# Optimization experiments

Measured on AMD Instinct MI355X. Metric: run time of the kernel, lower is better.

The kernel has to match this reference:

```python
import jax, jax.numpy as jnp
import numpy as np

B, T, D, V, L = 16, 1024, 512, 256, 64
INF = jnp.float32(1e30)


def _dp(reps, codebook):
    # per-frame squared L2 distance to each codebook token: (B, T, V)
    d = (jnp.sum(reps * reps, -1, keepdims=True)
         - 2.0 * jnp.einsum('btd,vd->btv', reps, codebook)
         + jnp.sum(codebook * codebook, -1))
    # cumulative cost table: C[:, t] = sum of distances of first t frames, C[:,0]=0
    C = jnp.concatenate([jnp.zeros((B, 1, V), d.dtype), jnp.cumsum(d, axis=1)], axis=1)

    def step(costs, t):
        start = jnp.maximum(t - L, 0)
        s_idx = start + jnp.arange(L)                          # candidate segment starts
        Ct = jax.lax.dynamic_slice(C, (0, t, 0), (B, 1, V))    # (B,1,V)
        Cw = jax.lax.dynamic_slice(C, (0, start, 0), (B, L, V))
        seg = Ct - Cw                                          # (B,L,V): cost of segment (s, t] per token
        seg_tok = jnp.argmin(seg, axis=-1)                     # best token per start
        seg_cost = jnp.take_along_axis(seg, seg_tok[..., None], axis=-1)[..., 0]
        cw = jax.lax.dynamic_slice(costs, (0, start), (B, L))
        total = jnp.where((s_idx < t)[None, :], cw + seg_cost, INF)
        idx = jnp.argmin(total, axis=1)                        # best start within window
        val = jnp.take_along_axis(total, idx[:, None], 1)[:, 0]
        tok = jnp.take_along_axis(seg_tok, idx[:, None], 1)[:, 0]
        prev = start + idx
        costs = jax.lax.dynamic_update_slice(costs, val[:, None], (0, t))
        return costs, (prev.astype(jnp.int32), tok.astype(jnp.int32))

    costs0 = jnp.zeros((B, T + 1), d.dtype)
    costs, (prev_t, tok_t) = jax.lax.scan(step, costs0, jnp.arange(1, T + 1))
    prev = jnp.zeros((B, T + 1), jnp.int32).at[:, 1:].set(prev_t.T)
    tokens = jnp.zeros((B, T + 1), jnp.int32).at[:, 1:].set(tok_t.T)
    return costs, prev, tokens


def _backtrack(prev, tokens, lengths):
    bidx = jnp.arange(B)

    def step(st, _):
        active = st > 0
        bnd = jnp.where(active, st, 0)
        tk = jnp.where(active, tokens[bidx, st], 0)
        st_new = jnp.where(active, prev[bidx, st], 0)
        return st_new, (bnd, tk, active)

    _, (bs, ts, act) = jax.lax.scan(step, lengths, None, length=T)
    bs, ts, act = bs.T, ts.T, act.T                            # (B,T), back-to-front order
    counts = jnp.sum(act.astype(jnp.int32), axis=1)
    ridx = counts[:, None] - 1 - jnp.arange(T)[None, :]        # reverse to front-to-back
    valid = ridx >= 0
    ridx = jnp.clip(ridx, 0, T - 1)
    boundaries = jnp.where(valid, jnp.take_along_axis(bs, ridx, 1), 0)
    label_tokens = jnp.where(valid, jnp.take_along_axis(ts, ridx, 1), 0)
    return boundaries, label_tokens, counts


def setup_inputs() -> dict:
    key = jax.random.key(0)
    k1, k2, k3 = jax.random.split(key, 3)
    reps = jax.random.normal(k1, (B, T, D), dtype=jnp.float32)
    codebook = jax.random.normal(k2, (V, D), dtype=jnp.float32)
    lengths = jax.random.randint(k3, (B,), T // 2, T + 1, dtype=jnp.int32)
    return {"reps": reps, "codebook": codebook, "lengths": lengths}


def reference(reps, codebook, lengths):
    lengths = jnp.minimum(lengths, T).astype(jnp.int32)
    costs, prev, tokens = _dp(reps, codebook)
    boundaries, label_tokens, counts = _backtrack(prev, tokens, lengths)
    final_costs = costs[jnp.arange(B), lengths]
    return boundaries, label_tokens, counts, final_costs
```

## Files before the change

kernel.cpp:

```cpp
#include <hip/hip_runtime.h>

#define BB 16
#define TT 1024
#define DD 512
#define VV 256
#define MM (BB*TT)

#define DPINF 1e30f

typedef __attribute__((ext_vector_type(8))) short bf16x8;
typedef __attribute__((ext_vector_type(4))) float f32x4;

#define DPP_MIN_STEP(m, CTRL) { \
  int _t = __builtin_amdgcn_update_dpp(__float_as_int(m), __float_as_int(m), CTRL, 0xF, 0xF, false); \
  m = fminf(m, __int_as_float(_t)); }

#define DPP_MIN_REDUCE(m) \
  DPP_MIN_STEP(m, 0x111); DPP_MIN_STEP(m, 0x112); DPP_MIN_STEP(m, 0x114); \
  DPP_MIN_STEP(m, 0x118); DPP_MIN_STEP(m, 0x142); DPP_MIN_STEP(m, 0x143);

__global__ __launch_bounds__(256) void fill_k(int4* __restrict__ Wf) {
  size_t i = (size_t)blockIdx.x * 256 + threadIdx.x;
  Wf[i] = make_int4(0x7F7F7F7F, 0x7F7F7F7F, 0x7F7F7F7F, 0x7F7F7F7F);
}

__global__ __launch_bounds__(256) void norms_k(const float* __restrict__ reps,
                                               const float* __restrict__ cb,
                                               float* __restrict__ r2,
                                               float* __restrict__ c2,
                                               ushort* __restrict__ repsb,
                                               ushort* __restrict__ cbb) {
  int row = blockIdx.x * 4 + (threadIdx.x >> 6);
  int lane = threadIdx.x & 63;
  const float* src;
  float* dst;
  ushort* bdst;
  if (row < MM) {
    src = reps + (size_t)row * DD;
    dst = r2 + row;
    bdst = repsb + (size_t)row * DD;
  } else {
    int r = row - MM;
    if (r >= VV) return;
    src = cb + (size_t)r * DD;
    dst = c2 + r;
    bdst = cbb + (size_t)r * DD;
  }
  const float4* s4 = (const float4*)src;
  float4 a = s4[lane];
  float4 b = s4[lane + 64];

  auto cvt = [](float x) -> ushort {
    unsigned u = __float_as_uint(x);
    return (ushort)((u + 0x7FFFu + ((u >> 16) & 1u)) >> 16);
  };
  ushort4 ua = make_ushort4(cvt(a.x), cvt(a.y), cvt(a.z), cvt(a.w));
  ushort4 ub = make_ushort4(cvt(b.x), cvt(b.y), cvt(b.z), cvt(b.w));
  *(ushort4*)&bdst[lane * 4] = ua;
  *(ushort4*)&bdst[256 + lane * 4] = ub;

  float s = a.x*a.x + a.y*a.y + a.z*a.z + a.w*a.w
          + b.x*b.x + b.y*b.y + b.z*b.z + b.w*b.w;
#pragma unroll
  for (int off = 1; off < 64; off <<= 1) s += __shfl_xor(s, off);
  if (lane == 0) *dst = s;
}

__global__ __launch_bounds__(256) void gemm_k(const ushort* __restrict__ repsb,
                                              const ushort* __restrict__ cbb,
                                              const float* __restrict__ r2,
                                              const float* __restrict__ c2,
                                              float* __restrict__ dmat) {
  __shared__ short Ab[2][4096];
  __shared__ short Bb[2][4096];
  int tid = threadIdx.x;
  int w = tid >> 6, l = tid & 63;
  int m0 = blockIdx.x * 64, v0 = blockIdx.y * 64;

  int srow = l >> 3;
  int scol = ((l & 7) << 4) ^ (srow << 4);

  auto stage = [&](int buf, int kc) {
#pragma unroll
    for (int ii = 0; ii < 2; ++ii) {
      int instr = w + ii * 4;
      int row = instr * 8 + srow;
      const char* ga = (const char*)repsb + ((size_t)(m0 + row) * DD + kc * 64) * 2 + scol;
      __builtin_amdgcn_global_load_lds((const unsigned int*)ga,
                                       (unsigned int*)&Ab[buf][instr * 512], 16, 0, 0);
      const char* gb = (const char*)cbb + ((size_t)(v0 + row) * DD + kc * 64) * 2 + scol;
      __builtin_amdgcn_global_load_lds((const unsigned int*)gb,
                                       (unsigned int*)&Bb[buf][instr * 512], 16, 0, 0);
    }
  };

  int fr = l & 15;
  int fq = l >> 4;
  int swz = (fr & 7) << 3;

  f32x4 acc0 = {0.f,0.f,0.f,0.f}, acc1 = {0.f,0.f,0.f,0.f};
  f32x4 acc2 = {0.f,0.f,0.f,0.f}, acc3 = {0.f,0.f,0.f,0.f};

  stage(0, 0);
  int cur = 0;
  for (int kc = 0; kc < 8; ++kc) {
    if (kc < 7) {
      stage(cur ^ 1, kc + 1);
      asm volatile("s_waitcnt vmcnt(4)" ::: "memory");
    } else {
      asm volatile("s_waitcnt vmcnt(0)" ::: "memory");
    }
    __syncthreads();
#pragma unroll
    for (int ks = 0; ks < 2; ++ks) {
      int koff = (ks * 32 + fq * 8) ^ swz;
      bf16x8 av = *(const bf16x8*)&Ab[cur][(w * 16 + fr) * 64 + koff];
      bf16x8 b0 = *(const bf16x8*)&Bb[cur][(0 * 16 + fr) * 64 + koff];
      bf16x8 b1 = *(const bf16x8*)&Bb[cur][(1 * 16 + fr) * 64 + koff];
      bf16x8 b2 = *(const bf16x8*)&Bb[cur][(2 * 16 + fr) * 64 + koff];
      bf16x8 b3 = *(const bf16x8*)&Bb[cur][(3 * 16 + fr) * 64 + koff];
      acc0 = __builtin_amdgcn_mfma_f32_16x16x32_bf16(av, b0, acc0, 0, 0, 0);
      acc1 = __builtin_amdgcn_mfma_f32_16x16x32_bf16(av, b1, acc1, 0, 0, 0);
      acc2 = __builtin_amdgcn_mfma_f32_16x16x32_bf16(av, b2, acc2, 0, 0, 0);
      acc3 = __builtin_amdgcn_mfma_f32_16x16x32_bf16(av, b3, acc3, 0, 0, 0);
    }
    __syncthreads();
    cur ^= 1;
  }

  float rv[4];
#pragma unroll
  for (int r = 0; r < 4; ++r) rv[r] = r2[m0 + w * 16 + fq * 4 + r];
#pragma unroll
  for (int vt = 0; vt < 4; ++vt) {
    f32x4 a = (vt == 0) ? acc0 : (vt == 1) ? acc1 : (vt == 2) ? acc2 : acc3;
    int v = v0 + vt * 16 + fr;
    float cc = c2[v];
#pragma unroll
    for (int r = 0; r < 4; ++r) {
      int m = m0 + w * 16 + fq * 4 + r;
      dmat[(size_t)m * VV + v] = fmaf(-2.f, a[r], rv[r] + cc);
    }
  }
}

__global__ __launch_bounds__(256, 4) void w_k(const float* __restrict__ dmat,
                                              int* __restrict__ Wf) {
  __shared__ __align__(16) float CL[128 * 64];
  __shared__ __align__(16) float TOT[16 * 64];
  int bx = blockIdx.x;
  int b = bx >> 6;
  int chunk = (bx >> 2) & 15;
  int q = bx & 3;
  int t1 = 1 + (chunk << 6);
  int tid = threadIdx.x;
  int wv = tid >> 6, lane = tid & 63;

  {
    int c = tid >> 4;
    int g = tid & 15;
    const float* base = dmat + (size_t)b * TT * VV + q * 64 + (g << 2);
    float4 rr[8];
    float4 run = make_float4(0.f, 0.f, 0.f, 0.f);
#pragma unroll
    for (int jj = 1; jj <= 8; ++jj) {
      int k = (c << 3) + jj;
      int f = t1 - 64 + k;
      bool valid = (k <= 127) && (f >= 1) && (f <= TT);
      int fc = valid ? f : 1;
      float4 dv = *(const float4*)(base + (size_t)(fc - 1) * VV);
      if (!valid) dv = make_float4(0.f, 0.f, 0.f, 0.f);
      run.x += dv.x; run.y += dv.y; run.z += dv.z; run.w += dv.w;
      rr[jj - 1] = run;
    }
    *(float4*)&TOT[(c << 6) + (g << 2)] = run;
    if (c == 0) *(float4*)&CL[(g << 2)] = make_float4(0.f, 0.f, 0.f, 0.f);
    __syncthreads();
    float4 off = make_float4(0.f, 0.f, 0.f, 0.f);
#pragma unroll
    for (int cc = 0; cc < 15; ++cc) {
      if (cc < c) {
        float4 tv = *(const float4*)&TOT[(cc << 6) + (g << 2)];
        off.x += tv.x; off.y += tv.y; off.z += tv.z; off.w += tv.w;
      }
    }
#pragma unroll
    for (int jj = 1; jj <= 8; ++jj) {
      int k = (c << 3) + jj;
      if (k <= 127) {
        float4 s = rr[jj - 1];
        s.x += off.x; s.y += off.y; s.z += off.z; s.w += off.w;
        *(float4*)&CL[(k << 6) + ((g ^ (k & 15)) << 2)] = s;
      }
    }
  }
  __syncthreads();

  float bw[16];
#pragma unroll
  for (int j = 0; j < 16; ++j) {
    int dt = (j << 2) + wv;
    int ks = dt + lane;
    int kt = dt + 64;
    int rti = __float_as_int(CL[(kt << 6) + (((lane >> 2) ^ (kt & 15)) << 2) + (lane & 3)]);
    int ksm = ks & 15;
    const float* rs = &CL[ks << 6];
    float bv = 1e38f;
#pragma unroll
    for (int g = 0; g < 16; ++g) {
      float4 a = *(const float4*)&rs[(g ^ ksm) << 2];
      int v0 = g << 2;
      float t0 = __int_as_float(__builtin_amdgcn_readlane(rti, v0));
      float t1v = __int_as_float(__builtin_amdgcn_readlane(rti, v0 + 1));
      float t2 = __int_as_float(__builtin_amdgcn_readlane(rti, v0 + 2));
      float t3 = __int_as_float(__builtin_amdgcn_readlane(rti, v0 + 3));
      float m01 = fminf(t0 - a.x, t1v - a.y);
      float m23 = fminf(t2 - a.z, t3 - a.w);
      bv = fminf(bv, fminf(m01, m23));
    }
    bw[j] = bv;
  }

  __syncthreads();
  float* ST = CL;
#pragma unroll
  for (int j = 0; j < 16; ++j) {
    int dt = (j << 2) + wv;
    int srow = dt + lane;
    ST[(63 - lane) * 127 + srow] = bw[j];
  }
  __syncthreads();
  {
    int* Wfb = Wf + (size_t)b * TT * 64;
    for (int qq = 0; qq < 32; ++qq) {
      int rr = wv * 32 + qq;
      if (rr > 126) break;
      int s = t1 - 64 + rr;
      if (s < 0) continue;
      int jlo = 63 - rr; if (jlo < 0) jlo = 0;
      int jhi = 126 - rr; if (jhi > 63) jhi = 63;
      int j = lane;
      if (j >= jlo && j <= jhi)
        atomicMin(&Wfb[(size_t)s * 64 + j], __float_as_int(ST[j * 127 + rr]));
    }
  }
}

__global__ __launch_bounds__(64) void dp_seq(const float* __restrict__ Wf,
                                             float* __restrict__ cg) {
  __shared__ __align__(16) float ring[256 * 64];
  int b = blockIdx.x;
  int lane = threadIdx.x;
  const char* Wb = (const char*)(Wf + (size_t)b * TT * 64);
  float* cgb = cg + (size_t)b * (TT + 1);
  if (lane == 0) cgb[0] = 0.f;

  auto stage4 = [&](int d) {
    const char* g = Wb + ((size_t)d << 10) + (lane << 4);
    __builtin_amdgcn_global_load_lds((const unsigned int*)g,
                                     (unsigned int*)&ring[((d << 2) & 255) << 6], 16, 0, 0);
  };
  auto ldring = [&](int r) -> float {
    int rc = (r > TT - 1) ? (TT - 1) : r;
    return ring[((rc & 255) << 6) | ((lane - rc) & 63)];
  };

  for (int d = 0; d < 60; ++d) stage4(d);
  asm volatile("s_waitcnt vmcnt(56)" ::: "memory");
  float p0 = ldring(0), p1 = ldring(1), p2 = ldring(2), p3 = ldring(3);
  float p4 = ldring(4), p5 = ldring(5), p6 = ldring(6), p7 = ldring(7);

  float c = 0.f;
  float acc = DPINF;
  float ckeep = 0.f;

#define STEP(TAU, P) { \
    float cand = c + (P); \
    acc = fminf(acc, cand); \
    int fl = (TAU) & 63; \
    float cnew = __int_as_float(__builtin_amdgcn_readlane(__float_as_int(acc), fl)); \
    bool me = (lane == fl); \
    ckeep = me ? cnew : ckeep; \
    acc = me ? DPINF : acc; \
    c = cnew; }

  for (int gg = 0; gg < 16; ++gg) {
#pragma unroll
    for (int ii = 0; ii < 8; ++ii) {
      int tb = gg * 64 + ii * 8;
      if (tb <= 776) {
        asm volatile("s_waitcnt vmcnt(56)" ::: "memory");
        stage4(60 + (tb >> 2)); stage4(61 + (tb >> 2));
      } else if (tb == 784) {
        asm volatile("s_waitcnt vmcnt(0)" ::: "memory");
      }
      STEP(tb + 0, p0); p0 = ldring(tb + 8);
      STEP(tb + 1, p1); p1 = ldring(tb + 9);
      STEP(tb + 2, p2); p2 = ldring(tb + 10);
      STEP(tb + 3, p3); p3 = ldring(tb + 11);
      STEP(tb + 4, p4); p4 = ldring(tb + 12);
      STEP(tb + 5, p5); p5 = ldring(tb + 13);
      STEP(tb + 6, p6); p6 = ldring(tb + 14);
      STEP(tb + 7, p7); p7 = ldring(tb + 15);
    }
    cgb[gg * 64 + 1 + lane] = ckeep;
  }
#undef STEP
}

__global__ __launch_bounds__(256) void prev_k(const float* __restrict__ Wf,
                                              const float* __restrict__ cg,
                                              int* __restrict__ pk) {
  __shared__ float WL[127 * 64];
  int bx = blockIdx.x;
  int b = bx >> 4;
  int chunk = bx & 15;
  int t0 = chunk << 6;
  int tid = threadIdx.x;
  int wv = tid >> 6, lane = tid & 63;

  const float* Wfb = Wf + (size_t)b * TT * 64;
  for (int ci = tid; ci < 127 * 16; ci += 256) {
    int row = ci >> 4, c4 = ci & 15;
    long s = (long)(t0 - 63 + row);
    float4 v = *(const float4*)(Wfb + s * 64 + (c4 << 2));
    *(float4*)&WL[(row << 6) + (c4 << 2)] = v;
  }
  __syncthreads();

  const float* cgb = cg + (size_t)b * (TT + 1);
#pragma unroll
  for (int u = 0; u < 16; ++u) {
    int tt = wv * 16 + u;
    int t = t0 + 1 + tt;
    int i = lane;
    int s = t - 64 + i;
    float wval = WL[(tt + i) * 64 + (63 - i)];
    int sc = (s < 0) ? 0 : s;
    float total = (s >= 0) ? (cgb[sc] + wval) : DPINF;
    float m = total;
    DPP_MIN_REDUCE(m);
    float mf = __int_as_float(__builtin_amdgcn_readlane(__float_as_int(m), 63));
    unsigned long long msk = __ballot(total == mf);
    int iwin = __builtin_ctzll(msk);
    int prev = t - 64 + iwin;
    if (lane == 0) pk[(size_t)b * (TT + 1) + t] = prev;
  }
}

__global__ __launch_bounds__(64) void bt_k(const int* __restrict__ pk,
                                           const float* __restrict__ cg,
                                           const int* __restrict__ lengths,
                                           float* __restrict__ out) {
  __shared__ ushort J[10][TT + 1];
  int b = blockIdx.x;
  int lane = threadIdx.x;
  const int* pb = pk + (size_t)b * (TT + 1);

  for (int t = lane; t <= TT; t += 64)
    J[0][t] = (ushort)((t == 0) ? 0 : pb[t]);
  __syncthreads();
#pragma unroll
  for (int k = 0; k < 9; ++k) {
    for (int t = lane; t <= TT; t += 64)
      J[k + 1][t] = J[k][J[k][t]];
    __syncthreads();
  }

  int len = lengths[b];
  len = (len > TT) ? TT : (len < 0 ? 0 : len);

  int cnt = 0;
  if (len > 0) {
    int cur = len, m = 0;
#pragma unroll
    for (int k = 9; k >= 0; --k) {
      int nxt = J[k][cur];
      if (nxt != 0) { cur = nxt; m += (1 << k); }
    }
    cnt = m + 1;
  }

  float* bout = out + b * TT;
  float* tout = out + MM + b * TT;
#pragma unroll 4
  for (int j0 = 0; j0 < TT; j0 += 64) {
    int j = j0 + lane;
    int node = 0;
    if (j < cnt) {
      int steps = cnt - 1 - j;
      int cur = len;
#pragma unroll
      for (int k = 9; k >= 0; --k)
        if ((steps >> k) & 1) cur = J[k][cur];
      node = cur;
    }
    bout[j] = (float)node;
    tout[j] = 0.f;
  }
  if (lane == 0) {
    out[2 * MM + b] = (float)cnt;
    out[2 * MM + BB + b] = cg[(size_t)b * (TT + 1) + len];
  }
}

__global__ __launch_bounds__(256) void tok_k(const float* __restrict__ dmat,
                                             float* __restrict__ out) {
  int bx = blockIdx.x;
  int b = bx >> 8;
  int wv = threadIdx.x >> 6, lane = threadIdx.x & 63;
  int j = ((bx & 255) << 2) + wv;
  int cnt = (int)out[2 * MM + b];
  if (j >= cnt) return;
  const float* bout = out + b * TT;
  int t = (int)bout[j];
  int s = (j == 0) ? 0 : (int)bout[j - 1];

  const float4* base = (const float4*)(dmat + (size_t)b * TT * VV);
  float4 acc = make_float4(0.f, 0.f, 0.f, 0.f);
  for (int f = s; f < t; ++f) {
    float4 dv = base[(size_t)f * 64 + lane];
    acc.x += dv.x; acc.y += dv.y; acc.z += dv.z; acc.w += dv.w;
  }
  float bv = acc.x; int be = 0;
  if (acc.y < bv) { bv = acc.y; be = 1; }
  if (acc.z < bv) { bv = acc.z; be = 2; }
  if (acc.w < bv) { bv = acc.w; be = 3; }
  float m = bv;
  DPP_MIN_REDUCE(m);
  float mf = __int_as_float(__builtin_amdgcn_readlane(__float_as_int(m), 63));
  unsigned long long msk = __ballot(bv == mf);
  int iwin = __builtin_ctzll(msk);
  int vloc = (lane << 2) + be;
  int v = __builtin_amdgcn_readlane(vloc, iwin);
  if (lane == 0) out[MM + b * TT + j] = (float)v;
}

extern "C" void kernel_launch(void* const* d_in, const int* in_sizes, int n_in,
                              void* d_out, int out_size, void* d_ws, size_t ws_size,
                              hipStream_t stream) {
  const float* reps = (const float*)d_in[0];
  const float* cb   = (const float*)d_in[1];
  const int* lengths = (const int*)d_in[2];
  float* out = (float*)d_out;

  char* ws = (char*)d_ws;
  float* r2 = (float*)ws;
  float* c2 = (float*)(ws + 65536);
  char* p = ws + 69632;
  float* dmat = (float*)p;               p += (size_t)MM * VV * 4;
  ushort* repsb = (ushort*)p;            p += (size_t)MM * DD * 2;
  float* cg   = (float*)p;               p += (size_t)BB * (TT + 1) * 4;
  int* pk     = (int*)p;                 p += (size_t)BB * (TT + 1) * 4;
  ushort* cbb = (ushort*)p;
  int* Wf = (int*)repsb;

  norms_k<<<(MM + VV) / 4, 256, 0, stream>>>(reps, cb, r2, c2, repsb, cbb);
  gemm_k<<<dim3(MM / 64, VV / 64), 256, 0, stream>>>(repsb, cbb, r2, c2, dmat);
  fill_k<<<(MM * 64 / 4) / 256, 256, 0, stream>>>((int4*)Wf);
  w_k<<<BB * 16 * 4, 256, 0, stream>>>(dmat, Wf);
  dp_seq<<<BB, 64, 0, stream>>>((const float*)Wf, cg);
  prev_k<<<BB * 16, 256, 0, stream>>>((const float*)Wf, cg, pk);
  bt_k<<<BB, 64, 0, stream>>>(pk, cg, lengths, out);
  tok_k<<<BB * 256, 256, 0, stream>>>(dmat, out);
}
```

Measured before the change: 124.8 us.

## Store distance matrix in bf16, fuse fill into norms, widen backtrack block

The distance matrix is written by the GEMM as bf16 instead of fp32, and the cumulative-cost and token kernels read it back as bf16. This halves the traffic of the largest intermediate buffer. The separate fill kernel is folded into norms_k as extra blocks, with Wf moved to its own workspace region, which removes one launch. The backtrack kernel goes from 64 to 256 threads. Rounding distances to bf16 before the cumulative sums can change argmin ties and segment choices, which risks mismatched outputs.

```diff
diff --git a/kernel.cpp b/kernel.cpp
--- a/kernel.cpp
+++ b/kernel.cpp
@@ -7,9 +7,19 @@
 #define MM (BB*TT)
 
 #define DPINF 1e30f
+#define NORM_BLOCKS ((MM + VV) / 4)
+#define FILL_BLOCKS 1024
 
 typedef __attribute__((ext_vector_type(8))) short bf16x8;
 typedef __attribute__((ext_vector_type(4))) float f32x4;
+
+__device__ __forceinline__ ushort f2bf(float x) {
+  unsigned u = __float_as_uint(x);
+  return (ushort)((u + 0x7FFFu + ((u >> 16) & 1u)) >> 16);
+}
+__device__ __forceinline__ float bf2f(ushort u) {
+  return __uint_as_float((unsigned)u << 16);
+}
 
 #define DPP_MIN_STEP(m, CTRL) { \
   int _t = __builtin_amdgcn_update_dpp(__float_as_int(m), __float_as_int(m), CTRL, 0xF, 0xF, false); \
@@ -18,18 +28,19 @@
 #define DPP_MIN_REDUCE(m) \
   DPP_MIN_STEP(m, 0x111); DPP_MIN_STEP(m, 0x112); DPP_MIN_STEP(m, 0x114); \
   DPP_MIN_STEP(m, 0x118); DPP_MIN_STEP(m, 0x142); DPP_MIN_STEP(m, 0x143);
-
-__global__ __launch_bounds__(256) void fill_k(int4* __restrict__ Wf) {
-  size_t i = (size_t)blockIdx.x * 256 + threadIdx.x;
-  Wf[i] = make_int4(0x7F7F7F7F, 0x7F7F7F7F, 0x7F7F7F7F, 0x7F7F7F7F);
-}
 
 __global__ __launch_bounds__(256) void norms_k(const float* __restrict__ reps,
                                                const float* __restrict__ cb,
                                                float* __restrict__ r2,
                                                float* __restrict__ c2,
                                                ushort* __restrict__ repsb,
-                                               ushort* __restrict__ cbb) {
+                                               ushort* __restrict__ cbb,
+                                               int4* __restrict__ Wf) {
+  if (blockIdx.x >= NORM_BLOCKS) {
+    size_t i = (size_t)(blockIdx.x - NORM_BLOCKS) * 256 + threadIdx.x;
+    Wf[i] = make_int4(0x7F7F7F7F, 0x7F7F7F7F, 0x7F7F7F7F, 0x7F7F7F7F);
+    return;
+  }
   int row = blockIdx.x * 4 + (threadIdx.x >> 6);
   int lane = threadIdx.x & 63;
   const float* src;
@@ -50,12 +61,8 @@
   float4 a = s4[lane];
   float4 b = s4[lane + 64];
 
-  auto cvt = [](float x) -> ushort {
-    unsigned u = __float_as_uint(x);
-    return (ushort)((u + 0x7FFFu + ((u >> 16) & 1u)) >> 16);
-  };
-  ushort4 ua = make_ushort4(cvt(a.x), cvt(a.y), cvt(a.z), cvt(a.w));
-  ushort4 ub = make_ushort4(cvt(b.x), cvt(b.y), cvt(b.z), cvt(b.w));
+  ushort4 ua = make_ushort4(f2bf(a.x), f2bf(a.y), f2bf(a.z), f2bf(a.w));
+  ushort4 ub = make_ushort4(f2bf(b.x), f2bf(b.y), f2bf(b.z), f2bf(b.w));
   *(ushort4*)&bdst[lane * 4] = ua;
   *(ushort4*)&bdst[256 + lane * 4] = ub;
 
@@ -70,7 +77,7 @@
                                               const ushort* __restrict__ cbb,
                                               const float* __restrict__ r2,
                                               const float* __restrict__ c2,
-                                              float* __restrict__ dmat) {
+                                              ushort* __restrict__ dmatb) {
   __shared__ short Ab[2][4096];
   __shared__ short Bb[2][4096];
   int tid = threadIdx.x;
@@ -139,12 +146,12 @@
 #pragma unroll
     for (int r = 0; r < 4; ++r) {
       int m = m0 + w * 16 + fq * 4 + r;
-      dmat[(size_t)m * VV + v] = fmaf(-2.f, a[r], rv[r] + cc);
-    }
-  }
-}
-
-__global__ __launch_bounds__(256, 4) void w_k(const float* __restrict__ dmat,
+      dmatb[(size_t)m * VV + v] = f2bf(fmaf(-2.f, a[r], rv[r] + cc));
+    }
+  }
+}
+
+__global__ __launch_bounds__(256, 4) void w_k(const ushort* __restrict__ dmatb,
                                               int* __restrict__ Wf) {
   __shared__ __align__(16) float CL[128 * 64];
   __shared__ __align__(16) float TOT[16 * 64];
@@ -159,7 +166,7 @@
   {
     int c = tid >> 4;
     int g = tid & 15;
-    const float* base = dmat + (size_t)b * TT * VV + q * 64 + (g << 2);
+    const ushort* base = dmatb + (size_t)b * TT * VV + q * 64 + (g << 2);
     float4 rr[8];
     float4 run = make_float4(0.f, 0.f, 0.f, 0.f);
 #pragma unroll
@@ -168,7 +175,8 @@
       int f = t1 - 64 + k;
       bool valid = (k <= 127) && (f >= 1) && (f <= TT);
       int fc = valid ? f : 1;
-      float4 dv = *(const float4*)(base + (size_t)(fc - 1) * VV);
+      ushort4 d4 = *(const ushort4*)(base + (size_t)(fc - 1) * VV);
+      float4 dv = make_float4(bf2f(d4.x), bf2f(d4.y), bf2f(d4.z), bf2f(d4.w));
       if (!valid) dv = make_float4(0.f, 0.f, 0.f, 0.f);
       run.x += dv.x; run.y += dv.y; run.z += dv.z; run.w += dv.w;
       rr[jj - 1] = run;
@@ -348,21 +356,21 @@
   }
 }
 
-__global__ __launch_bounds__(64) void bt_k(const int* __restrict__ pk,
-                                           const float* __restrict__ cg,
-                                           const int* __restrict__ lengths,
-                                           float* __restrict__ out) {
+__global__ __launch_bounds__(256) void bt_k(const int* __restrict__ pk,
+                                            const float* __restrict__ cg,
+                                            const int* __restrict__ lengths,
+                                            float* __restrict__ out) {
   __shared__ ushort J[10][TT + 1];
   int b = blockIdx.x;
-  int lane = threadIdx.x;
+  int tid = threadIdx.x;
   const int* pb = pk + (size_t)b * (TT + 1);
 
-  for (int t = lane; t <= TT; t += 64)
+  for (int t = tid; t <= TT; t += 256)
     J[0][t] = (ushort)((t == 0) ? 0 : pb[t]);
   __syncthreads();
 #pragma unroll
   for (int k = 0; k < 9; ++k) {
-    for (int t = lane; t <= TT; t += 64)
+    for (int t = tid; t <= TT; t += 256)
       J[k + 1][t] = J[k][J[k][t]];
     __syncthreads();
   }
@@ -383,9 +391,9 @@
 
   float* bout = out + b * TT;
   float* tout = out + MM + b * TT;
-#pragma unroll 4
-  for (int j0 = 0; j0 < TT; j0 += 64) {
-    int j = j0 + lane;
+#pragma unroll
+  for (int j0 = 0; j0 < TT; j0 += 256) {
+    int j = j0 + tid;
     int node = 0;
     if (j < cnt) {
       int steps = cnt - 1 - j;
@@ -398,13 +406,13 @@
     bout[j] = (float)node;
     tout[j] = 0.f;
   }
-  if (lane == 0) {
+  if (tid == 0) {
     out[2 * MM + b] = (float)cnt;
     out[2 * MM + BB + b] = cg[(size_t)b * (TT + 1) + len];
   }
 }
 
-__global__ __launch_bounds__(256) void tok_k(const float* __restrict__ dmat,
+__global__ __launch_bounds__(256) void tok_k(const ushort* __restrict__ dmatb,
                                              float* __restrict__ out) {
   int bx = blockIdx.x;
   int b = bx >> 8;
@@ -416,11 +424,12 @@
   int t = (int)bout[j];
   int s = (j == 0) ? 0 : (int)bout[j - 1];
 
-  const float4* base = (const float4*)(dmat + (size_t)b * TT * VV);
+  const ushort* base = dmatb + (size_t)b * TT * VV + lane * 4;
   float4 acc = make_float4(0.f, 0.f, 0.f, 0.f);
   for (int f = s; f < t; ++f) {
-    float4 dv = base[(size_t)f * 64 + lane];
-    acc.x += dv.x; acc.y += dv.y; acc.z += dv.z; acc.w += dv.w;
+    ushort4 d4 = *(const ushort4*)(base + (size_t)f * VV);
+    acc.x += bf2f(d4.x); acc.y += bf2f(d4.y);
+    acc.z += bf2f(d4.z); acc.w += bf2f(d4.w);
   }
   float bv = acc.x; int be = 0;
   if (acc.y < bv) { bv = acc.y; be = 1; }
@@ -448,19 +457,19 @@
   float* r2 = (float*)ws;
   float* c2 = (float*)(ws + 65536);
   char* p = ws + 69632;
-  float* dmat = (float*)p;               p += (size_t)MM * VV * 4;
+  ushort* dmatb = (ushort*)p;            p += (size_t)MM * VV * 2;
   ushort* repsb = (ushort*)p;            p += (size_t)MM * DD * 2;
+  int* Wf     = (int*)p;                 p += (size_t)MM * 64 * 4;
   float* cg   = (float*)p;               p += (size_t)BB * (TT + 1) * 4;
   int* pk     = (int*)p;                 p += (size_t)BB * (TT + 1) * 4;
   ushort* cbb = (ushort*)p;
-  int* Wf = (int*)repsb;
-
-  norms_k<<<(MM + VV) / 4, 256, 0, stream>>>(reps, cb, r2, c2, repsb, cbb);
-  gemm_k<<<dim3(MM / 64, VV / 64), 256, 0, stream>>>(repsb, cbb, r2, c2, dmat);
-  fill_k<<<(MM * 64 / 4) / 256, 256, 0, stream>>>((int4*)Wf);
-  w_k<<<BB * 16 * 4, 256, 0, stream>>>(dmat, Wf);
+
+  norms_k<<<NORM_BLOCKS + FILL_BLOCKS, 256, 0, stream>>>(reps, cb, r2, c2,
+                                                         repsb, cbb, (int4*)Wf);
+  gemm_k<<<dim3(MM / 64, VV / 64), 256, 0, stream>>>(repsb, cbb, r2, c2, dmatb);
+  w_k<<<BB * 16 * 4, 256, 0, stream>>>(dmatb, Wf);
   dp_seq<<<BB, 64, 0, stream>>>((const float*)Wf, cg);
   prev_k<<<BB * 16, 256, 0, stream>>>((const float*)Wf, cg, pk);
-  bt_k<<<BB, 64, 0, stream>>>(pk, cg, lengths, out);
-  tok_k<<<BB * 256, 256, 0, stream>>>(dmat, out);
-}
+  bt_k<<<BB, 256, 0, stream>>>(pk, cg, lengths, out);
+  tok_k<<<BB * 256, 256, 0, stream>>>(dmatb, out);
+}
```

Result: faster. 106.6 us, median of 2 (-14.6%).
